# Kernel optimization log

Measured on AMD Instinct MI355X. Metric: run time of the kernel, lower is better.

## Reference

```python
import jax, jax.numpy as jnp
import numpy as np

GD, D, S, L = 14, 128, 16, 2  # gaussian_dim, hidden_dim, d_state, num_layers


def _layernorm(x, g, b):
    m = x.mean(-1, keepdims=True)
    v = ((x - m) ** 2).mean(-1, keepdims=True)
    return (x - m) / jnp.sqrt(v + 1e-5) * g + b


def _scan_dir(x, dtW, dtb, BW, CW, Alog, Dskip):
    # x: [M, N, D]. Diagonal selective SSM, one direction.
    dt = jax.nn.softplus(x @ dtW + dtb)          # [M, N, D]
    Bm = x @ BW                                   # [M, N, S]
    Cm = x @ CW                                   # [M, N, S]
    A = -jnp.exp(Alog)                            # [D, S]

    def step(s, inp):
        x_t, dt_t, B_t, C_t = inp                 # [M,D],[M,D],[M,S],[M,S]
        s = jnp.exp(A * dt_t[:, :, None]) * s + (dt_t * x_t)[:, :, None] * B_t[:, None, :]
        y = jnp.einsum('mds,ms->md', s, C_t) + Dskip * x_t
        return s, y

    s0 = jnp.zeros((x.shape[0], D, S), x.dtype)
    _, ys = jax.lax.scan(step, s0, (x.transpose(1, 0, 2), dt.transpose(1, 0, 2),
                                    Bm.transpose(1, 0, 2), Cm.transpose(1, 0, 2)))
    return ys.transpose(1, 0, 2)                  # [M, N, D]


def setup_inputs() -> dict:
    key = jax.random.key(0)
    ks = jax.random.split(key, 20)
    N, B, P = 8, 1, 20000
    inp = {}
    inp['xyz'] = jax.random.normal(ks[0], (N, B, P, 3), jnp.float32)
    inp['scale'] = jax.random.normal(ks[1], (N, B, P, 3), jnp.float32)
    inp['rotation'] = jax.random.normal(ks[2], (N, B, P, 4), jnp.float32)
    inp['opacity'] = jax.random.normal(ks[3], (N, B, P, 1), jnp.float32)
    inp['color'] = jax.random.normal(ks[4], (N, B, P, 3), jnp.float32)
    inp['t'] = jnp.array([0.37], jnp.float32)
    inp['timestamps'] = jnp.linspace(0.0, 1.0, N, dtype=jnp.float32)

    def lin(k, i, o):
        return (jax.random.normal(k, (i, o), jnp.float32) / np.sqrt(i)).astype(jnp.float32)

    inp['in_W'] = lin(ks[5], GD, D); inp['in_b'] = jnp.zeros((D,), jnp.float32)
    inp['ln_g'] = jnp.ones((L, D), jnp.float32); inp['ln_b'] = jnp.zeros((L, D), jnp.float32)
    inp['dt_W'] = jax.random.normal(ks[6], (L, 2, D, D), jnp.float32) / np.sqrt(D)
    inp['dt_b'] = jnp.zeros((L, 2, D), jnp.float32)
    inp['B_W'] = jax.random.normal(ks[7], (L, 2, D, S), jnp.float32) / np.sqrt(D)
    inp['C_W'] = jax.random.normal(ks[8], (L, 2, D, S), jnp.float32) / np.sqrt(D)
    inp['A_log'] = jnp.log(jax.random.uniform(ks[9], (L, 2, D, S), jnp.float32, 0.5, 2.0))
    inp['D_skip'] = jnp.ones((L, 2, D), jnp.float32)
    inp['out_W'] = jax.random.normal(ks[10], (L, 2 * D, D), jnp.float32) / np.sqrt(2 * D)
    inp['out_b'] = jnp.zeros((L, D), jnp.float32)
    inp['te_W1'] = jax.random.normal(ks[11], (1, D), jnp.float32)
    inp['te_b1'] = jnp.zeros((D,), jnp.float32)
    inp['te_W2'] = jax.random.normal(ks[12], (D, D), jnp.float32) / np.sqrt(D)
    inp['te_b2'] = jnp.zeros((D,), jnp.float32)
    inp['op_W'] = jax.random.normal(ks[13], (D, GD), jnp.float32) / np.sqrt(D)
    inp['op_b'] = jnp.zeros((GD,), jnp.float32)
    return inp


def reference(xyz, scale, rotation, opacity, color, t, timestamps,
              in_W, in_b, ln_g, ln_b, dt_W, dt_b, B_W, C_W, A_log, D_skip,
              out_W, out_b, te_W1, te_b1, te_W2, te_b2, op_W, op_b):
    N, B, P = xyz.shape[0], xyz.shape[1], xyz.shape[2]
    M = B * P
    # stack frames: [N,B,P,14] -> [B*P, N, 14]
    params = jnp.concatenate([xyz, scale, rotation, opacity, color], -1)
    params = params.transpose(1, 2, 0, 3).reshape(M, N, GD)
    h = params @ in_W + in_b                      # [M, N, D]
    # sinusoidal temporal position encoding from continuous timestamps
    ts = jnp.broadcast_to(timestamps[None, :], (M, N))
    half = D // 2
    freqs = jnp.exp(-jnp.log(10000.0) * jnp.arange(half, dtype=h.dtype) / half)
    ang = ts[..., None] * freqs                   # [M, N, D/2]
    h = h + jnp.concatenate([jnp.sin(ang), jnp.cos(ang)], -1)
    # bidirectional SSM layers (pre-LN, residual)
    for l in range(L):
        xn = _layernorm(h, ln_g[l], ln_b[l])
        yf = _scan_dir(xn, dt_W[l, 0], dt_b[l, 0], B_W[l, 0], C_W[l, 0], A_log[l, 0], D_skip[l, 0])
        yb = jnp.flip(_scan_dir(jnp.flip(xn, 1), dt_W[l, 1], dt_b[l, 1], B_W[l, 1], C_W[l, 1],
                                A_log[l, 1], D_skip[l, 1]), 1)
        h = h + jnp.concatenate([yf, yb], -1) @ out_W[l] + out_b[l]
    # temporal query: linear interpolation between neighboring hidden states
    t_full = jnp.broadcast_to(t.reshape(B, 1), (B, P)).reshape(M)
    tn = t_full * (N - 1)
    idx_low = jnp.clip(jnp.floor(tn).astype(jnp.int32), 0, N - 2)
    idx_high = jnp.minimum(idx_low + 1, N - 1)
    alpha = (tn - idx_low.astype(h.dtype))[:, None]
    rows = jnp.arange(M)
    h_low = h[rows, idx_low]                      # [M, D]
    h_high = h[rows, idx_high]
    h_i = (1.0 - alpha) * h_low + alpha * h_high
    te = jax.nn.silu(t_full[:, None] @ te_W1 + te_b1) @ te_W2 + te_b2
    h_i = h_i + te
    out = (h_i @ op_W + op_b).reshape(B, P, GD)
    xyz_o = out[..., :3]
    scale_o = jax.nn.softplus(out[..., 3:6])
    rot = out[..., 6:10]
    rot_o = rot / jnp.clip(jnp.linalg.norm(rot, axis=-1, keepdims=True), 1e-12)
    opac_o = jax.nn.sigmoid(out[..., 10:11])
    col_o = jax.nn.sigmoid(out[..., 11:14])
    # dict fields concatenated in canonical order -> [B, P, 14]
    return jnp.concatenate([xyz_o, scale_o, rot_o, opac_o, col_o], -1)
```

## Files before the change

kernel.cpp:

```cpp
#include <hip/hip_runtime.h>
#include <math.h>

#define DD   128
#define SS   16
#define NL   2
#define GDIM 14
#define NN   8

typedef short  s16x8 __attribute__((ext_vector_type(8)));
typedef float  f32x4 __attribute__((ext_vector_type(4)));
typedef unsigned short ushort_t;

#define WS_INW   0
#define WS_DTW   4096
#define WS_BCW   69632
#define WS_OUTW  86016
#define WS_USH   151552
#define WS_AFLT  8192

#if __has_builtin(__builtin_amdgcn_exp2f)
#define EXP2(x) __builtin_amdgcn_exp2f(x)
#else
#define EXP2(x) exp2f(x)
#endif

__device__ __forceinline__ unsigned short f2bf(float f) {
    unsigned u = __float_as_uint(f);
    u += 0x7fffu + ((u >> 16) & 1u);
    return (unsigned short)(u >> 16);
}

__device__ __forceinline__ float softplus_fast(float x) {
    return fmaxf(x, 0.f) + __logf(1.f + __expf(-fabsf(x)));
}
__device__ __forceinline__ float softplus_precise(float x) {
    return fmaxf(x, 0.f) + log1pf(expf(-fabsf(x)));
}

extern "C" __global__ void __launch_bounds__(256)
prep_weights(const float* __restrict__ inW, const float* __restrict__ dtW,
             const float* __restrict__ BW,  const float* __restrict__ CW,
             const float* __restrict__ outW, const float* __restrict__ Alog,
             ushort_t* __restrict__ ws)
{
    int i = blockIdx.x * 256 + threadIdx.x;
    if (i < 4096) {
        int d = i >> 5, k = i & 31;
        ws[WS_INW + i] = (k < GDIM) ? f2bf(inW[k * DD + d]) : (ushort_t)0;
        return;
    }
    i -= 4096;
    if (i < 65536) {
        int l = i >> 15, r = i & 32767;
        int col = r >> 7, k = r & 127;
        int dir = col >> 7, d = col & 127;
        ws[WS_DTW + i] = f2bf(dtW[((size_t)(l * 2 + dir) * DD + k) * DD + d]);
        return;
    }
    i -= 65536;
    if (i < 16384) {
        int l = i >> 13, r = i & 8191;
        int col = r >> 7, k = r & 127;
        int dir = col >> 5, which = (col >> 4) & 1, s = col & 15;
        const float* Wsrc = which ? CW : BW;
        ws[WS_BCW + i] = f2bf(Wsrc[((size_t)(l * 2 + dir) * DD + k) * SS + s]);
        return;
    }
    i -= 16384;
    if (i < 65536) {
        int l = i >> 15, r = i & 32767;
        int col = r >> 8, k = r & 255;
        ws[WS_OUTW + i] = f2bf(outW[((size_t)l * 2 * DD + k) * DD + col]);
        return;
    }
    i -= 65536;
    if (i < WS_AFLT) {
        float* wsf = (float*)(ws + WS_USH);
        int ld = i >> 11, r = i & 2047;
        int s = r >> 7, d = r & 127;
        wsf[i] = -expf(Alog[((size_t)ld * DD + d) * SS + s]) * 1.44269504088896f;
    }
}

extern "C" __global__ void __launch_bounds__(256, 4)
ssm_mfma(const float* __restrict__ xyz, const float* __restrict__ scl,
         const float* __restrict__ rotp, const float* __restrict__ opa,
         const float* __restrict__ colp,
         const float* __restrict__ t_arr, const float* __restrict__ tstamp,
         const float* __restrict__ inB,
         const float* __restrict__ lnG, const float* __restrict__ lnB,
         const float* __restrict__ dtB,
         const float* __restrict__ Dskp,
         const float* __restrict__ outB,
         const float* __restrict__ teW1, const float* __restrict__ teB1,
         const float* __restrict__ teW2, const float* __restrict__ teB2,
         const float* __restrict__ opW, const float* __restrict__ opB,
         const ushort_t* __restrict__ wsu,
         float* __restrict__ out, int M, int Pb)
{
    const int t    = threadIdx.x;
    const int lane = t & 63;
    const int wv   = t >> 6;
    const int d    = t & 127;
    const int p    = t >> 7;
    const int m0   = blockIdx.x * 2;
    const int m    = m0 + p;
    const int r16  = lane & 15;
    const int kg   = lane >> 4;

    __shared__ float arenaA[16][132];
    __shared__ float arenaB[16][260];
    __shared__ float bcres[16][68];
    __shared__ float red  [4][2][NN];
    __shared__ float vec  [2][128];
    __shared__ float hi2  [2][132];
    __shared__ float outg [2][16];

    float (*pres)[132] = arenaA;
    ushort_t* XsU = (ushort_t*)&arenaA[0][0];
    float (*dtres)[260] = arenaB;
    ushort_t* YsU = (ushort_t*)&arenaB[0][0];

    const ushort_t* inWt  = wsu + WS_INW;
    const ushort_t* dtWt  = wsu + WS_DTW;
    const ushort_t* bcWt  = wsu + WS_BCW;
    const ushort_t* outWt = wsu + WS_OUTW;
    const float*    Apre  = (const float*)(wsu + WS_USH);

    for (int idx = t; idx < 16 * 32; idx += 256) {
        const int row = idx >> 5, k = idx & 31;
        const int pp = row >> 3, n = row & 7;
        const int mm = m0 + pp;
        float v = 0.f;
        if (k < GDIM && mm < M) {
            if (k < 3)       v = xyz [((size_t)n * M + mm) * 3 + k];
            else if (k < 6)  v = scl [((size_t)n * M + mm) * 3 + (k - 3)];
            else if (k < 10) v = rotp[((size_t)n * M + mm) * 4 + (k - 6)];
            else if (k < 11) v = opa [ (size_t)n * M + mm];
            else             v = colp[((size_t)n * M + mm) * 3 + (k - 11)];
        }
        XsU[row * 264 + k] = f2bf(v);
    }
    __syncthreads();

    {
        const s16x8 a = *(const s16x8*)&XsU[r16 * 264 + kg * 8];
        __syncthreads();
        #pragma unroll
        for (int ti = 0; ti < 2; ++ti) {
            const int col = (wv * 2 + ti) * 16 + r16;
            const s16x8 b = *(const s16x8*)&inWt[col * 32 + kg * 8];
            f32x4 acc = {0.f, 0.f, 0.f, 0.f};
            acc = __builtin_amdgcn_mfma_f32_16x16x32_bf16(a, b, acc, 0, 0, 0);
            #pragma unroll
            for (int j = 0; j < 4; ++j) pres[kg * 4 + j][col] = acc[j];
        }
    }
    __syncthreads();

    float h[NN];
    {
        const float hb = inB[d];
        const int j = d & 63;
        const float freq = EXP2(-13.2877123795f * (float)j * (1.f / 64.f));
        #pragma unroll
        for (int n = 0; n < NN; ++n) {
            const float ang = tstamp[n] * freq;
            h[n] = pres[p * 8 + n][d] + hb + ((d < 64) ? __sinf(ang) : __cosf(ang));
        }
    }

    for (int l = 0; l < NL; ++l) {
        float sum[NN], sq[NN];
        #pragma unroll
        for (int n = 0; n < NN; ++n) { sum[n] = h[n]; sq[n] = h[n] * h[n]; }
        #pragma unroll
        for (int off = 32; off > 0; off >>= 1) {
            #pragma unroll
            for (int n = 0; n < NN; ++n) {
                sum[n] += __shfl_xor(sum[n], off);
                sq[n]  += __shfl_xor(sq[n],  off);
            }
        }
        if (lane == 0) {
            #pragma unroll
            for (int n = 0; n < NN; ++n) { red[wv][0][n] = sum[n]; red[wv][1][n] = sq[n]; }
        }
        __syncthreads();

        float xn[NN];
        {
            const float gg = lnG[l * DD + d], bb = lnB[l * DD + d];
            #pragma unroll
            for (int n = 0; n < NN; ++n) {
                const float s0 = red[2 * p][0][n] + red[2 * p + 1][0][n];
                const float s1 = red[2 * p][1][n] + red[2 * p + 1][1][n];
                const float mean = s0 * (1.f / 128.f);
                float var = s1 * (1.f / 128.f) - mean * mean;
                const float inv = rsqrtf(fmaxf(var, 0.f) + 1e-5f);
                xn[n] = fmaf((h[n] - mean) * inv, gg, bb);
                XsU[(p * 8 + n) * 264 + d] = f2bf(xn[n]);
            }
        }
        __syncthreads();

        {
            s16x8 a[4];
            #pragma unroll
            for (int kc = 0; kc < 4; ++kc)
                a[kc] = *(const s16x8*)&XsU[r16 * 264 + kc * 32 + kg * 8];

            const ushort_t* dtl = dtWt + l * 32768;
            #pragma unroll
            for (int ti = 0; ti < 4; ++ti) {
                const int col = (wv * 4 + ti) * 16 + r16;
                f32x4 acc = {0.f, 0.f, 0.f, 0.f};
                #pragma unroll
                for (int kc = 0; kc < 4; ++kc) {
                    const s16x8 b = *(const s16x8*)&dtl[col * 128 + kc * 32 + kg * 8];
                    acc = __builtin_amdgcn_mfma_f32_16x16x32_bf16(a[kc], b, acc, 0, 0, 0);
                }
                #pragma unroll
                for (int j = 0; j < 4; ++j) dtres[kg * 4 + j][col] = acc[j];
            }
            const ushort_t* bcl = bcWt + l * 8192;
            {
                const int col = wv * 16 + r16;
                f32x4 acc = {0.f, 0.f, 0.f, 0.f};
                #pragma unroll
                for (int kc = 0; kc < 4; ++kc) {
                    const s16x8 b = *(const s16x8*)&bcl[col * 128 + kc * 32 + kg * 8];
                    acc = __builtin_amdgcn_mfma_f32_16x16x32_bf16(a[kc], b, acc, 0, 0, 0);
                }
                #pragma unroll
                for (int j = 0; j < 4; ++j) bcres[kg * 4 + j][col] = acc[j];
            }
        }
        __syncthreads();

        float dtv[2][NN];
        #pragma unroll
        for (int dir = 0; dir < 2; ++dir) {
            const float db = dtB[(l * 2 + dir) * DD + d];
            #pragma unroll
            for (int n = 0; n < NN; ++n)
                dtv[dir][n] = softplus_fast(dtres[p * 8 + n][dir * 128 + d] + db);
        }
        __syncthreads();

        #pragma unroll
        for (int dir = 0; dir < 2; ++dir) {
            const float* Ap = Apre + (size_t)(l * 2 + dir) * SS * DD + d;
            float Ar[SS];
            #pragma unroll
            for (int s = 0; s < SS; ++s) Ar[s] = Ap[s * DD];
            const float dsk = Dskp[(l * 2 + dir) * DD + d];
            float st[SS];
            #pragma unroll
            for (int s = 0; s < SS; ++s) st[s] = 0.f;
            #pragma unroll
            for (int t8 = 0; t8 < NN; ++t8) {
                const int n = dir ? (NN - 1 - t8) : t8;
                const float dtc = dtv[dir][n];
                const float xv  = xn[n];
                const float dx  = dtc * xv;
                float y = dsk * xv;
                const float* base = &bcres[p * 8 + n][dir * 32];
                #pragma unroll
                for (int s4 = 0; s4 < SS; s4 += 4) {
                    const float4 Bv = *(const float4*)&base[s4];
                    const float4 Cv = *(const float4*)&base[16 + s4];
                    st[s4+0] = fmaf(EXP2(Ar[s4+0] * dtc), st[s4+0], dx * Bv.x);
                    y = fmaf(st[s4+0], Cv.x, y);
                    st[s4+1] = fmaf(EXP2(Ar[s4+1] * dtc), st[s4+1], dx * Bv.y);
                    y = fmaf(st[s4+1], Cv.y, y);
                    st[s4+2] = fmaf(EXP2(Ar[s4+2] * dtc), st[s4+2], dx * Bv.z);
                    y = fmaf(st[s4+2], Cv.z, y);
                    st[s4+3] = fmaf(EXP2(Ar[s4+3] * dtc), st[s4+3], dx * Bv.w);
                    y = fmaf(st[s4+3], Cv.w, y);
                }
                YsU[(p * 8 + n) * 520 + dir * 128 + d] = f2bf(y);
            }
        }
        __syncthreads();

        {
            s16x8 a[8];
            #pragma unroll
            for (int kc = 0; kc < 8; ++kc)
                a[kc] = *(const s16x8*)&YsU[r16 * 520 + kc * 32 + kg * 8];
            const ushort_t* ol = outWt + l * 32768;
            #pragma unroll
            for (int ti = 0; ti < 2; ++ti) {
                const int col = (wv * 2 + ti) * 16 + r16;
                f32x4 acc = {0.f, 0.f, 0.f, 0.f};
                #pragma unroll
                for (int kc = 0; kc < 8; ++kc) {
                    const s16x8 b = *(const s16x8*)&ol[col * 256 + kc * 32 + kg * 8];
                    acc = __builtin_amdgcn_mfma_f32_16x16x32_bf16(a[kc], b, acc, 0, 0, 0);
                }
                #pragma unroll
                for (int j = 0; j < 4; ++j) pres[kg * 4 + j][col] = acc[j];
            }
        }
        __syncthreads();

        {
            const float ob = outB[l * DD + d];
            #pragma unroll
            for (int n = 0; n < NN; ++n) h[n] += pres[p * 8 + n][d] + ob;
        }
    }

    const int mc = (m < M) ? m : (M - 1);
    const float tv = t_arr[mc / Pb];
    const float tn = tv * (float)(NN - 1);
    int il = (int)floorf(tn);
    il = il < 0 ? 0 : (il > NN - 2 ? NN - 2 : il);
    const float alpha = tn - (float)il;
    float hlow = 0.f, hhigh = 0.f;
    #pragma unroll
    for (int n = 0; n < NN; ++n) {
        if (n == il)     hlow  = h[n];
        if (n == il + 1) hhigh = h[n];
    }
    float hi = (1.f - alpha) * hlow + alpha * hhigh;

    {
        const float u = fmaf(tv, teW1[d], teB1[d]);
        vec[p][d] = u / (1.f + __expf(-u));
    }
    __syncthreads();
    {
        float acc = teB2[d];
        for (int k = 0; k < DD; k += 4) {
            const float4 s4 = *(const float4*)&vec[p][k];
            acc = fmaf(s4.x, teW2[(k + 0) * DD + d], acc);
            acc = fmaf(s4.y, teW2[(k + 1) * DD + d], acc);
            acc = fmaf(s4.z, teW2[(k + 2) * DD + d], acc);
            acc = fmaf(s4.w, teW2[(k + 3) * DD + d], acc);
        }
        hi += acc;
    }
    __syncthreads();
    hi2[p][d] = hi;
    __syncthreads();

    if (d < GDIM * 8) {
        const int g = d >> 3, j = d & 7;
        float part = 0.f;
        #pragma unroll
        for (int q = 0; q < 16; ++q)
            part = fmaf(hi2[p][j + 8 * q], opW[(j + 8 * q) * GDIM + g], part);
        part += __shfl_xor(part, 4);
        part += __shfl_xor(part, 2);
        part += __shfl_xor(part, 1);
        if (j == 0) outg[p][g] = part + opB[g];
    }
    __syncthreads();

    if (d < GDIM && m < M) {
        const int g = d;
        const float v = outg[p][g];
        float r;
        if (g < 3)        r = v;
        else if (g < 6)   r = softplus_precise(v);
        else if (g < 10) {
            const float q0 = outg[p][6], q1 = outg[p][7], q2 = outg[p][8], q3 = outg[p][9];
            const float nrm = sqrtf(fmaf(q0,q0, fmaf(q1,q1, fmaf(q2,q2, q3*q3))));
            r = v / fmaxf(nrm, 1e-12f);
        } else {
            r = 1.f / (1.f + expf(-v));
        }
        out[(size_t)m * GDIM + g] = r;
    }
}

extern "C" void kernel_launch(void* const* d_in, const int* in_sizes, int n_in,
                              void* d_out, int out_size, void* d_ws, size_t ws_size,
                              hipStream_t stream) {
    const float* xyz   = (const float*)d_in[0];
    const float* scl   = (const float*)d_in[1];
    const float* rotp  = (const float*)d_in[2];
    const float* opa   = (const float*)d_in[3];
    const float* colp  = (const float*)d_in[4];
    const float* t_arr = (const float*)d_in[5];
    const float* tstmp = (const float*)d_in[6];
    const float* inW   = (const float*)d_in[7];
    const float* inB   = (const float*)d_in[8];
    const float* lnG   = (const float*)d_in[9];
    const float* lnB   = (const float*)d_in[10];
    const float* dtW   = (const float*)d_in[11];
    const float* dtB   = (const float*)d_in[12];
    const float* BW    = (const float*)d_in[13];
    const float* CW    = (const float*)d_in[14];
    const float* Alog  = (const float*)d_in[15];
    const float* Dskp  = (const float*)d_in[16];
    const float* outW  = (const float*)d_in[17];
    const float* outB  = (const float*)d_in[18];
    const float* teW1  = (const float*)d_in[19];
    const float* teB1  = (const float*)d_in[20];
    const float* teW2  = (const float*)d_in[21];
    const float* teB2  = (const float*)d_in[22];
    const float* opW   = (const float*)d_in[23];
    const float* opB   = (const float*)d_in[24];

    const int N  = in_sizes[6];
    const int M  = in_sizes[3] / N;
    const int B  = in_sizes[5];
    const int Pb = M / B;
    (void)out_size; (void)n_in;

    ushort_t* wsu = (ushort_t*)d_ws;
    const int prep_elems = WS_USH + WS_AFLT;
    hipLaunchKernelGGL(prep_weights, dim3((prep_elems + 255) / 256), dim3(256), 0, stream,
                       inW, dtW, BW, CW, outW, Alog, wsu);
    hipLaunchKernelGGL(ssm_mfma, dim3((M + 1) / 2), dim3(256), 0, stream,
                       xyz, scl, rotp, opa, colp, t_arr, tstmp,
                       inB, lnG, lnB, dtB, Dskp, outB,
                       teW1, teB1, teW2, teB2, opW, opB,
                       wsu, (float*)d_out, M, Pb);
}
```

Before: 517.1 us.

## Precompute positional and time embeddings in prep kernel, shrink LDS for occupancy

Moves the sinusoidal positional embedding plus input bias, and the per-batch time-embedding MLP, out of the per-block kernel into the weight-prep kernel, so each block only loads precomputed vectors. It aliases the bcres, vec, hi2 and outg shared arrays onto the existing arenas, which cuts LDS use, and raises the launch-bounds occupancy hint from 4 to 6 blocks per CU. An extra barrier is added after the A-fragment loads so the aliased arena can be overwritten safely. The higher occupancy target may force register spills.

```diff
diff --git a/kernel.cpp b/kernel.cpp
--- a/kernel.cpp
+++ b/kernel.cpp
@@ -17,6 +17,8 @@
 #define WS_OUTW  86016
 #define WS_USH   151552
 #define WS_AFLT  8192
+#define WS_PEB   8192
+#define WS_TE    9216
 
 #if __has_builtin(__builtin_amdgcn_exp2f)
 #define EXP2(x) __builtin_amdgcn_exp2f(x)
@@ -41,8 +43,13 @@
 prep_weights(const float* __restrict__ inW, const float* __restrict__ dtW,
              const float* __restrict__ BW,  const float* __restrict__ CW,
              const float* __restrict__ outW, const float* __restrict__ Alog,
-             ushort_t* __restrict__ ws)
+             const float* __restrict__ tstamp, const float* __restrict__ inB,
+             const float* __restrict__ t_arr,
+             const float* __restrict__ teW1, const float* __restrict__ teB1,
+             const float* __restrict__ teW2, const float* __restrict__ teB2,
+             int Bcnt, ushort_t* __restrict__ ws)
 {
+    float* wsf = (float*)(ws + WS_USH);
     int i = blockIdx.x * 256 + threadIdx.x;
     if (i < 4096) {
         int d = i >> 5, k = i & 31;
@@ -75,25 +82,43 @@
     }
     i -= 65536;
     if (i < WS_AFLT) {
-        float* wsf = (float*)(ws + WS_USH);
         int ld = i >> 11, r = i & 2047;
         int s = r >> 7, d = r & 127;
         wsf[i] = -expf(Alog[((size_t)ld * DD + d) * SS + s]) * 1.44269504088896f;
-    }
-}
-
-extern "C" __global__ void __launch_bounds__(256, 4)
+        return;
+    }
+    i -= WS_AFLT;
+    if (i < 1024) {
+        int n = i >> 7, d = i & 127;
+        int j = d & 63;
+        float freq = expf(-logf(10000.f) * (float)j * (1.f / 64.f));
+        float ang = tstamp[n] * freq;
+        wsf[WS_PEB + i] = inB[d] + ((d < 64) ? sinf(ang) : cosf(ang));
+        return;
+    }
+    i -= 1024;
+    if (i < Bcnt * 128) {
+        int b = i >> 7, d = i & 127;
+        float tv = t_arr[b];
+        float acc = teB2[d];
+        for (int k = 0; k < DD; ++k) {
+            float u = fmaf(tv, teW1[k], teB1[k]);
+            float s = u / (1.f + expf(-u));
+            acc = fmaf(s, teW2[k * DD + d], acc);
+        }
+        wsf[WS_TE + i] = acc;
+    }
+}
+
+extern "C" __global__ void __launch_bounds__(256, 6)
 ssm_mfma(const float* __restrict__ xyz, const float* __restrict__ scl,
          const float* __restrict__ rotp, const float* __restrict__ opa,
          const float* __restrict__ colp,
-         const float* __restrict__ t_arr, const float* __restrict__ tstamp,
-         const float* __restrict__ inB,
+         const float* __restrict__ t_arr,
          const float* __restrict__ lnG, const float* __restrict__ lnB,
          const float* __restrict__ dtB,
          const float* __restrict__ Dskp,
          const float* __restrict__ outB,
-         const float* __restrict__ teW1, const float* __restrict__ teB1,
-         const float* __restrict__ teW2, const float* __restrict__ teB2,
          const float* __restrict__ opW, const float* __restrict__ opB,
          const ushort_t* __restrict__ wsu,
          float* __restrict__ out, int M, int Pb)
@@ -110,14 +135,11 @@
 
     __shared__ float arenaA[16][132];
     __shared__ float arenaB[16][260];
-    __shared__ float bcres[16][68];
     __shared__ float red  [4][2][NN];
-    __shared__ float vec  [2][128];
-    __shared__ float hi2  [2][132];
-    __shared__ float outg [2][16];
 
     float (*pres)[132] = arenaA;
     ushort_t* XsU = (ushort_t*)&arenaA[0][0];
+    float (*bcres)[68] = (float(*)[68])&arenaA[0][0];
     float (*dtres)[260] = arenaB;
     ushort_t* YsU = (ushort_t*)&arenaB[0][0];
 
@@ -125,7 +147,10 @@
     const ushort_t* dtWt  = wsu + WS_DTW;
     const ushort_t* bcWt  = wsu + WS_BCW;
     const ushort_t* outWt = wsu + WS_OUTW;
-    const float*    Apre  = (const float*)(wsu + WS_USH);
+    const float*    wsf   = (const float*)(wsu + WS_USH);
+    const float*    Apre  = wsf;
+    const float*    peb   = wsf + WS_PEB;
+    const float*    te    = wsf + WS_TE;
 
     for (int idx = t; idx < 16 * 32; idx += 256) {
         const int row = idx >> 5, k = idx & 31;
@@ -159,16 +184,9 @@
     __syncthreads();
 
     float h[NN];
-    {
-        const float hb = inB[d];
-        const int j = d & 63;
-        const float freq = EXP2(-13.2877123795f * (float)j * (1.f / 64.f));
-        #pragma unroll
-        for (int n = 0; n < NN; ++n) {
-            const float ang = tstamp[n] * freq;
-            h[n] = pres[p * 8 + n][d] + hb + ((d < 64) ? __sinf(ang) : __cosf(ang));
-        }
-    }
+    #pragma unroll
+    for (int n = 0; n < NN; ++n)
+        h[n] = pres[p * 8 + n][d] + peb[n * DD + d];
 
     for (int l = 0; l < NL; ++l) {
         float sum[NN], sq[NN];
@@ -209,6 +227,7 @@
             #pragma unroll
             for (int kc = 0; kc < 4; ++kc)
                 a[kc] = *(const s16x8*)&XsU[r16 * 264 + kc * 32 + kg * 8];
+            __syncthreads();
 
             const ushort_t* dtl = dtWt + l * 32768;
             #pragma unroll
@@ -313,7 +332,8 @@
     }
 
     const int mc = (m < M) ? m : (M - 1);
-    const float tv = t_arr[mc / Pb];
+    const int bidx = mc / Pb;
+    const float tv = t_arr[bidx];
     const float tn = tv * (float)(NN - 1);
     int il = (int)floorf(tn);
     il = il < 0 ? 0 : (il > NN - 2 ? NN - 2 : il);
@@ -324,26 +344,10 @@
         if (n == il)     hlow  = h[n];
         if (n == il + 1) hhigh = h[n];
     }
-    float hi = (1.f - alpha) * hlow + alpha * hhigh;
-
-    {
-        const float u = fmaf(tv, teW1[d], teB1[d]);
-        vec[p][d] = u / (1.f + __expf(-u));
-    }
-    __syncthreads();
-    {
-        float acc = teB2[d];
-        for (int k = 0; k < DD; k += 4) {
-            const float4 s4 = *(const float4*)&vec[p][k];
-            acc = fmaf(s4.x, teW2[(k + 0) * DD + d], acc);
-            acc = fmaf(s4.y, teW2[(k + 1) * DD + d], acc);
-            acc = fmaf(s4.z, teW2[(k + 2) * DD + d], acc);
-            acc = fmaf(s4.w, teW2[(k + 3) * DD + d], acc);
-        }
-        hi += acc;
-    }
-    __syncthreads();
-    hi2[p][d] = hi;
+    float hi = (1.f - alpha) * hlow + alpha * hhigh + te[bidx * DD + d];
+
+    float* epi = &arenaB[0][0];
+    epi[p * 132 + d] = hi;
     __syncthreads();
 
     if (d < GDIM * 8) {
@@ -351,22 +355,23 @@
         float part = 0.f;
         #pragma unroll
         for (int q = 0; q < 16; ++q)
-            part = fmaf(hi2[p][j + 8 * q], opW[(j + 8 * q) * GDIM + g], part);
+            part = fmaf(epi[p * 132 + j + 8 * q], opW[(j + 8 * q) * GDIM + g], part);
         part += __shfl_xor(part, 4);
         part += __shfl_xor(part, 2);
         part += __shfl_xor(part, 1);
-        if (j == 0) outg[p][g] = part + opB[g];
+        if (j == 0) epi[264 + p * 16 + g] = part + opB[g];
     }
     __syncthreads();
 
     if (d < GDIM && m < M) {
         const int g = d;
-        const float v = outg[p][g];
+        const float v = epi[264 + p * 16 + g];
         float r;
         if (g < 3)        r = v;
         else if (g < 6)   r = softplus_precise(v);
         else if (g < 10) {
-            const float q0 = outg[p][6], q1 = outg[p][7], q2 = outg[p][8], q3 = outg[p][9];
+            const float q0 = epi[264 + p * 16 + 6], q1 = epi[264 + p * 16 + 7];
+            const float q2 = epi[264 + p * 16 + 8], q3 = epi[264 + p * 16 + 9];
             const float nrm = sqrtf(fmaf(q0,q0, fmaf(q1,q1, fmaf(q2,q2, q3*q3))));
             r = v / fmaxf(nrm, 1e-12f);
         } else {
@@ -412,12 +417,12 @@
     (void)out_size; (void)n_in;
 
     ushort_t* wsu = (ushort_t*)d_ws;
-    const int prep_elems = WS_USH + WS_AFLT;
+    const int prep_elems = WS_USH + WS_AFLT + 1024 + B * 128;
     hipLaunchKernelGGL(prep_weights, dim3((prep_elems + 255) / 256), dim3(256), 0, stream,
-                       inW, dtW, BW, CW, outW, Alog, wsu);
+                       inW, dtW, BW, CW, outW, Alog, tstmp, inB, t_arr,
+                       teW1, teB1, teW2, teB2, B, wsu);
     hipLaunchKernelGGL(ssm_mfma, dim3((M + 1) / 2), dim3(256), 0, stream,
-                       xyz, scl, rotp, opa, colp, t_arr, tstmp,
-                       inB, lnG, lnB, dtB, Dskp, outB,
-                       teW1, teB1, teW2, teB2, opW, opB,
+                       xyz, scl, rotp, opa, colp, t_arr,
+                       lnG, lnB, dtB, Dskp, outB, opW, opB,
                        wsu, (float*)d_out, M, Pb);
 }
```

Result: slower. 566.1 us (+9.5%).
